# Kernel tuning notes

Measured on AMD Instinct MI355X. Metric: run time of the kernel, lower is better.

The kernel has to match this reference:

```python
import jax, jax.numpy as jnp
import numpy as np

K_NN = 64          # ume_knn
RADIUS = 1.5       # ume_desc_rad
EPS_M = 1e-6
EPS_T = 1e-16


def ball_query_idx(kp, pts, K, radius):
    # kp: [bs, n_kp, 3], pts: [bs, N, 3] -> idx [bs, n_kp, K], -1 padded
    N = pts.shape[1]
    d2 = jnp.sum((kp[:, :, None, :] - pts[:, None, :, :]) ** 2, axis=-1)  # [bs,n_kp,N]
    mask = d2 < radius ** 2
    cand = jnp.where(mask, jnp.arange(N, dtype=jnp.int32), N)
    order = jnp.sort(cand, axis=-1)[..., :K]          # first K in-ball indices (by point index)
    return jnp.where(order == N, -1, order)


def ball_query_gather(pts, idx):
    # pad row 0 with zeros so idx=-1 gathers zeros (matches torch ball_query_gather)
    bs = pts.shape[0]
    padded = jnp.concatenate([jnp.zeros((bs, 1, pts.shape[-1]), pts.dtype), pts], axis=1)
    return padded[jnp.arange(bs)[:, None, None], idx + 1]  # [bs, n_kp, K, D]


def ume_mat(points, features):
    # points: [B', K, 3], features: [B', K, F] -> [B', F, 4]
    m0 = jnp.sum(features, axis=1)                       # [B', F]
    m1 = jnp.einsum('bkf,bkd->bfd', features, points)    # [B', F, 3]
    um = jnp.concatenate([m0[:, :, None], m1], axis=2)   # [B', F, 4]
    denom = jnp.sum(m0, axis=-1)[:, None, None] + EPS_M  # [B',1,1]
    return um / denom


def batch_estimate_transform_ume(G, H):
    # G, H: [B, F, 4]
    mg, mh = G[:, :, 0:1], H[:, :, 0:1]                  # [B,F,1]
    g, h = G[:, :, 1:], H[:, :, 1:]                      # [B,F,3]
    mg_sq = jnp.sum(mg ** 2, axis=1, keepdims=True) + EPS_T
    mg_mh = jnp.sum(mg * mh, axis=1, keepdims=True)
    gmg = jnp.sum(g * mg, axis=1, keepdims=True)         # [B,1,3]
    hmg = jnp.sum(h * mg, axis=1, keepdims=True)
    wlc = gmg / (mg_sq + EPS_T)
    wrc = hmg / (mg_mh + EPS_T)
    left = g - wlc * mg
    right = h - wrc * mh
    M = jnp.einsum('bfi,bfj->bij', right, left)          # right^T @ left, [B,3,3]
    U, S, VH = jnp.linalg.svd(jnp.swapaxes(M, 1, 2))
    sgn = jnp.sign(jnp.linalg.det(U @ VH))
    qd = jnp.stack([jnp.ones_like(sgn), jnp.ones_like(sgn), sgn], axis=-1)  # diag(1,1,sgn)
    R = (U * qd[:, None, :]) @ VH                        # [B,3,3]
    b2 = (wrc - wlc @ R)[:, 0, :]                        # [B,3]
    H_orth = jnp.linalg.qr(H, mode='reduced')[0]
    G_orth = jnp.linalg.qr(G, mode='reduced')[0]
    diff = H_orth @ jnp.swapaxes(H_orth, 1, 2) - G_orth @ jnp.swapaxes(G_orth, 1, 2)
    D = 0.707 * jnp.sqrt(jnp.sum(diff ** 2, axis=(1, 2)))
    top = jnp.concatenate([jnp.swapaxes(R, 1, 2), b2[:, :, None]], axis=2)  # [B,3,4]
    bottom = jnp.broadcast_to(jnp.array([[0.0, 0.0, 0.0, 1.0]], G.dtype), (G.shape[0], 1, 4))
    T = jnp.concatenate([top, bottom], axis=1)           # [B,4,4]
    return T, D


def setup_inputs() -> dict:
    key = jax.random.key(0)
    ks = jax.random.split(key, 6)
    bs, N, F, n_kp = 2, 16384, 64, 64
    return {
        'source_points': jax.random.normal(ks[0], (bs, N, 3), jnp.float32),
        'source_features': jax.random.uniform(ks[1], (bs, N, F), jnp.float32),
        'source_kp': jax.random.normal(ks[2], (bs, n_kp, 3), jnp.float32),
        'target_points': jax.random.normal(ks[3], (bs, N, 3), jnp.float32),
        'target_features': jax.random.uniform(ks[4], (bs, N, F), jnp.float32),
        'target_kp': jax.random.normal(ks[5], (bs, n_kp, 3), jnp.float32),
    }


def reference(source_points, source_features, source_kp, target_points, target_features, target_kp):
    bs, n_kp = source_kp.shape[0], source_kp.shape[1]
    F = source_features.shape[-1]
    s_idx = ball_query_idx(source_kp, source_points, K_NN, RADIUS)
    t_idx = ball_query_idx(target_kp, target_points, K_NN, RADIUS)
    s_pts = ball_query_gather(source_points, s_idx).reshape(bs * n_kp, K_NN, 3)
    s_ft = ball_query_gather(source_features, s_idx).reshape(bs * n_kp, K_NN, F)
    t_pts = ball_query_gather(target_points, t_idx).reshape(bs * n_kp, K_NN, 3)
    t_ft = ball_query_gather(target_features, t_idx).reshape(bs * n_kp, K_NN, F)
    G_kp = ume_mat(s_pts, s_ft).reshape(bs, n_kp, F, 4)[:, :, None]   # [bs,n_kp,1,F,4]
    H_kp = ume_mat(t_pts, t_ft).reshape(bs, n_kp, F, 4)[:, None]      # [bs,1,n_kp,F,4]
    G = jnp.broadcast_to(G_kp, (bs, n_kp, n_kp, F, 4)).reshape(-1, F, 4)
    H = jnp.broadcast_to(H_kp, (bs, n_kp, n_kp, F, 4)).reshape(-1, F, 4)
    T, D = batch_estimate_transform_ume(G, H)
    T = T.reshape(bs, n_kp, n_kp, 4, 4)
    D = D.reshape(bs, n_kp, n_kp)
    return T, D, jnp.squeeze(G_kp), jnp.squeeze(H_kp)
```

## Files before the change

### kernel.cpp

```cpp
#include <hip/hip_runtime.h>
#include <math.h>

#define N_PTS 16384
#define N_KP  64
#define NF    64
#define KNN   64
#define NWAVE 16

#define OFF_T 0
#define OFF_D 131072
#define OFF_G 139264
#define OFF_H 172032

__device__ __forceinline__ float wsum(float v) {
  #pragma unroll
  for (int m = 1; m < 64; m <<= 1) v += __shfl_xor(v, m, 64);
  return v;
}

__global__ __launch_bounds__(1024) void ume_stage1(
    const float* __restrict__ sp, const float* __restrict__ sf, const float* __restrict__ skp,
    const float* __restrict__ tp, const float* __restrict__ tf, const float* __restrict__ tkp,
    float* __restrict__ out, double* __restrict__ rec)
{
  const int kp = blockIdx.x, b = blockIdx.y, side = blockIdx.z;
  const int tid  = threadIdx.x;
  const int lane = tid & 63;
  const int w    = tid >> 6;
  const float* pts  = side ? tp  : sp;
  const float* feat = side ? tf  : sf;
  const float* kps  = side ? tkp : skp;

  const float kx = kps[(b*N_KP + kp)*3 + 0];
  const float ky = kps[(b*N_KP + kp)*3 + 1];
  const float kz = kps[(b*N_KP + kp)*3 + 2];

  __shared__ int   s_widx[NWAVE*KNN];
  __shared__ float s_wpx[NWAVE*KNN], s_wpy[NWAVE*KNN], s_wpz[NWAVE*KNN];
  __shared__ int   s_wcount[NWAVE];
  __shared__ int   s_woff[NWAVE];
  __shared__ int   s_total;
  __shared__ int   s_final[KNN];
  __shared__ float s_px[KNN], s_py[KNN], s_pz[KNN];
  __shared__ float s_m0[NWAVE][NF], s_mx[NWAVE][NF], s_my[NWAVE][NF], s_mz[NWAVE][NF];

  const float* base = pts + ((size_t)b*N_PTS + w*1024 + lane)*3;
  float cx = base[0], cy = base[1], cz = base[2];
  int running = 0;
  #pragma unroll 5
  for (int k = 0; k < 15; ++k) {
    const float* q = base + (size_t)(k+1)*192;
    const float nx = q[0], ny = q[1], nz = q[2];
    const float dx = cx-kx, dy = cy-ky, dz = cz-kz;
    const bool hit = (dx*dx + dy*dy + dz*dz) < 2.25f;
    const unsigned long long m = __ballot(hit);
    if (hit) {
      const int pos = running + __popcll(m & ((1ull<<lane)-1ull));
      if (pos < KNN) {
        s_widx[w*KNN + pos] = w*1024 + k*64 + lane;
        s_wpx[w*KNN + pos] = cx; s_wpy[w*KNN + pos] = cy; s_wpz[w*KNN + pos] = cz;
      }
    }
    running += (int)__popcll(m);
    cx = nx; cy = ny; cz = nz;
  }
  {
    const float dx = cx-kx, dy = cy-ky, dz = cz-kz;
    const bool hit = (dx*dx + dy*dy + dz*dz) < 2.25f;
    const unsigned long long m = __ballot(hit);
    if (hit) {
      const int pos = running + __popcll(m & ((1ull<<lane)-1ull));
      if (pos < KNN) {
        s_widx[w*KNN + pos] = w*1024 + 15*64 + lane;
        s_wpx[w*KNN + pos] = cx; s_wpy[w*KNN + pos] = cy; s_wpz[w*KNN + pos] = cz;
      }
    }
    running += (int)__popcll(m);
  }
  if (lane == 0) s_wcount[w] = running > KNN ? KNN : running;
  __syncthreads();

  if (tid < NWAVE) {
    int off = 0;
    for (int q = 0; q < tid; ++q) off += s_wcount[q];
    s_woff[tid] = off;
    if (tid == NWAVE-1) {
      int tot = off + s_wcount[tid];
      s_total = tot > KNN ? KNN : tot;
    }
  }
  __syncthreads();

  {
    const int e = tid & 63, ww = tid >> 6;
    if (e < s_wcount[ww]) {
      const int slot = s_woff[ww] + e;
      if (slot < KNN) {
        s_final[slot] = s_widx[ww*KNN + e];
        s_px[slot] = s_wpx[ww*KNN + e];
        s_py[slot] = s_wpy[ww*KNN + e];
        s_pz[slot] = s_wpz[ww*KNN + e];
      }
    }
  }
  __syncthreads();

  const int total = s_total;

  {
    const int f = tid & 63, g = tid >> 6;
    float m0 = 0.f, mxv = 0.f, myv = 0.f, mzv = 0.f;
    #pragma unroll
    for (int t = 0; t < 4; ++t) {
      const int k = g + t*NWAVE;
      if (k < total) {
        const float fv = feat[((size_t)b*N_PTS + s_final[k])*NF + f];
        m0  += fv;
        mxv += fv * s_px[k];
        myv += fv * s_py[k];
        mzv += fv * s_pz[k];
      }
    }
    s_m0[g][f] = m0; s_mx[g][f] = mxv; s_my[g][f] = myv; s_mz[g][f] = mzv;
  }
  __syncthreads();

  if (tid >= 64) return;

  float m0 = 0.f, mxv = 0.f, myv = 0.f, mzv = 0.f;
  #pragma unroll
  for (int g = 0; g < NWAVE; ++g) {
    m0  += s_m0[g][lane];
    mxv += s_mx[g][lane];
    myv += s_my[g][lane];
    mzv += s_mz[g][lane];
  }
  const float denom = wsum(m0) + 1e-6f;
  float u[4];
  u[0] = m0/denom; u[1] = mxv/denom; u[2] = myv/denom; u[3] = mzv/denom;

  float* dst = out + (side ? OFF_H : OFF_G) + ((size_t)(b*N_KP+kp)*NF + lane)*4;
  dst[0]=u[0]; dst[1]=u[1]; dst[2]=u[2]; dst[3]=u[3];

  float A[4][4];
  #pragma unroll
  for (int c = 0; c < 4; ++c)
    #pragma unroll
    for (int d = c; d < 4; ++d) {
      const float s = wsum(u[c]*u[d]);
      A[c][d] = s; A[d][c] = s;
    }

  if (lane < 16)
    rec[(size_t)((side*2 + b)*N_KP + kp)*16 + lane] = (double)A[lane>>2][lane&3];
}

__device__ __forceinline__ void chol_inv4(const double A[4][4], double Ai[4][4], double sc[4]) {
  #pragma unroll
  for (int c = 0; c < 4; ++c) sc[c] = 1.0/sqrt(fmax(A[c][c], 1e-300));
  double Ah[4][4];
  #pragma unroll
  for (int c = 0; c < 4; ++c)
    #pragma unroll
    for (int d = 0; d < 4; ++d) Ah[c][d] = A[c][d]*sc[c]*sc[d];
  double L[4][4] = {};
  for (int c = 0; c < 4; ++c) {
    double dv = Ah[c][c];
    for (int k = 0; k < c; ++k) dv -= L[c][k]*L[c][k];
    dv = sqrt(fmax(dv, 1e-14));
    L[c][c] = dv;
    for (int r = c+1; r < 4; ++r) {
      double v = Ah[r][c];
      for (int k = 0; k < c; ++k) v -= L[r][k]*L[c][k];
      L[r][c] = v/dv;
    }
  }
  double Li[4][4] = {};
  for (int c = 0; c < 4; ++c) {
    Li[c][c] = 1.0/L[c][c];
    for (int r = c+1; r < 4; ++r) {
      double s = 0.0;
      for (int k = c; k < r; ++k) s += L[r][k]*Li[k][c];
      Li[r][c] = -s/L[r][r];
    }
  }
  for (int r = 0; r < 4; ++r)
    for (int c = 0; c < 4; ++c) {
      double s = 0.0;
      for (int k = 0; k < 4; ++k) s += Li[k][r]*Li[k][c];
      Ai[r][c] = s;
    }
}

__global__ __launch_bounds__(64) void ume_stage2(
    const float* __restrict__ gh, float* __restrict__ out,
    const double* __restrict__ rec)
{
  const int jt = blockIdx.x, it = blockIdx.y, b = blockIdx.z;
  const int lane = threadIdx.x;
  const int i = it*8 + (lane >> 3);
  const int j = jt*8 + (lane & 7);

  const float4* Gp = (const float4*)(gh + OFF_G) + (size_t)(b*N_KP + i)*NF;
  const float4* Hp = (const float4*)(gh + OFF_H) + (size_t)(b*N_KP + j)*NF;

  double X[4][4] = {};
  for (int f = 0; f < NF; ++f) {
    const float4 g = Gp[f];
    const float4 h = Hp[f];
    const double gc[4] = {(double)g.x, (double)g.y, (double)g.z, (double)g.w};
    const double hc[4] = {(double)h.x, (double)h.y, (double)h.z, (double)h.w};
    #pragma unroll
    for (int c = 0; c < 4; ++c)
      #pragma unroll
      for (int d = 0; d < 4; ++d)
        X[c][d] += hc[c]*gc[d];
  }

  double Ag[4][4], Bh[4][4];
  {
    const double* pg = rec + (size_t)(b*N_KP + i)*16;
    const double* ph = rec + (size_t)((2 + b)*N_KP + j)*16;
    #pragma unroll
    for (int k = 0; k < 16; ++k) { Ag[k>>2][k&3] = pg[k]; Bh[k>>2][k&3] = ph[k]; }
  }
  double Aig[4][4], scg[4], Bih[4][4], sch[4];
  chol_inv4(Ag, Aig, scg);
  chol_inv4(Bh, Bih, sch);

  const double dwl = Ag[0][0] + 2e-16;
  const double wl[3] = {Ag[0][1]/dwl, Ag[0][2]/dwl, Ag[0][3]/dwl};
  const double dmm = X[0][0] + 1e-16;
  double wr[3];
  wr[0] = X[1][0]/dmm; wr[1] = X[2][0]/dmm; wr[2] = X[3][0]/dmm;

  double M[3][3];
  #pragma unroll
  for (int r = 0; r < 3; ++r)
    #pragma unroll
    for (int c = 0; c < 3; ++c)
      M[r][c] = X[1+r][1+c] - wl[c]*X[1+r][0] - wr[r]*X[0][1+c] + wr[r]*wl[c]*X[0][0];

  double C[3][3];
  for (int r = 0; r < 3; ++r)
    for (int c = 0; c < 3; ++c) C[r][c] = M[c][r];

  double mmax = 0.0;
  for (int r = 0; r < 3; ++r)
    for (int c = 0; c < 3; ++c) mmax = fmax(mmax, fabs(C[r][c]));

  double R[3][3] = {{1,0,0},{0,1,0},{0,0,1}};
  if (mmax > 1e-300) {
    const double is = 1.0/mmax;
    for (int r = 0; r < 3; ++r)
      for (int c = 0; c < 3; ++c) C[r][c] *= is;
    double K[3][3];
    for (int p = 0; p < 3; ++p)
      for (int q = 0; q < 3; ++q) {
        double s = 0.0;
        for (int r = 0; r < 3; ++r) s += C[r][p]*C[r][q];
        K[p][q] = s;
      }
    double V[3][3] = {{1,0,0},{0,1,0},{0,0,1}};
    for (int sweep = 0; sweep < 5; ++sweep) {
      for (int p = 0; p < 2; ++p)
        for (int q = p+1; q < 3; ++q) {
          const double apq = K[p][q];
          if (fabs(apq) < 1e-60) continue;
          const double tau = (K[q][q] - K[p][p])/(2.0*apq);
          const double t   = (tau >= 0.0 ? 1.0 : -1.0)/(fabs(tau) + sqrt(1.0 + tau*tau));
          const double cth = 1.0/sqrt(1.0 + t*t);
          const double sth = t*cth;
          for (int k = 0; k < 3; ++k) {
            const double a = K[p][k], bb_ = K[q][k];
            K[p][k] = cth*a - sth*bb_;
            K[q][k] = sth*a + cth*bb_;
          }
          for (int k = 0; k < 3; ++k) {
            const double a = K[k][p], bb_ = K[k][q];
            K[k][p] = cth*a - sth*bb_;
            K[k][q] = sth*a + cth*bb_;
          }
          for (int k = 0; k < 3; ++k) {
            const double a = V[k][p], bb_ = V[k][q];
            V[k][p] = cth*a - sth*bb_;
            V[k][q] = sth*a + cth*bb_;
          }
        }
    }
    int o0 = 0, o1 = 1, o2 = 2;
    double e0 = K[0][0], e1 = K[1][1], e2 = K[2][2];
    if (e0 < e1) { double te=e0; e0=e1; e1=te; int to=o0; o0=o1; o1=to; }
    if (e0 < e2) { double te=e0; e0=e2; e2=te; int to=o0; o0=o2; o2=to; }
    if (e1 < e2) { double te=e1; e1=e2; e2=te; int to=o1; o1=o2; o2=to; }
    (void)e0; (void)e1; (void)e2;
    double v1[3] = {V[0][o0], V[1][o0], V[2][o0]};
    double v2[3] = {V[0][o1], V[1][o1], V[2][o1]};
    double u1[3], u2[3];
    for (int r = 0; r < 3; ++r) u1[r] = C[r][0]*v1[0] + C[r][1]*v1[1] + C[r][2]*v1[2];
    const double n1 = sqrt(u1[0]*u1[0] + u1[1]*u1[1] + u1[2]*u1[2]);
    if (n1 > 1e-150) { u1[0]/=n1; u1[1]/=n1; u1[2]/=n1; }
    else             { u1[0]=1.0; u1[1]=0.0; u1[2]=0.0; }
    for (int r = 0; r < 3; ++r) u2[r] = C[r][0]*v2[0] + C[r][1]*v2[1] + C[r][2]*v2[2];
    const double d12 = u2[0]*u1[0] + u2[1]*u1[1] + u2[2]*u1[2];
    for (int r = 0; r < 3; ++r) u2[r] -= d12*u1[r];
    const double n2 = sqrt(u2[0]*u2[0] + u2[1]*u2[1] + u2[2]*u2[2]);
    if (n2 > 1e-100) { u2[0]/=n2; u2[1]/=n2; u2[2]/=n2; }
    else {
      double t0, t1, t2;
      if (fabs(u1[0]) < 0.9) { t0=1.0; t1=0.0; t2=0.0; } else { t0=0.0; t1=1.0; t2=0.0; }
      const double dd = t0*u1[0] + t1*u1[1] + t2*u1[2];
      u2[0]=t0-dd*u1[0]; u2[1]=t1-dd*u1[1]; u2[2]=t2-dd*u1[2];
      const double nn = sqrt(u2[0]*u2[0] + u2[1]*u2[1] + u2[2]*u2[2]);
      u2[0]/=nn; u2[1]/=nn; u2[2]/=nn;
    }
    const double u3[3] = {u1[1]*u2[2]-u1[2]*u2[1], u1[2]*u2[0]-u1[0]*u2[2], u1[0]*u2[1]-u1[1]*u2[0]};
    const double v3[3] = {v1[1]*v2[2]-v1[2]*v2[1], v1[2]*v2[0]-v1[0]*v2[2], v1[0]*v2[1]-v1[1]*v2[0]};
    for (int r = 0; r < 3; ++r)
      for (int c = 0; c < 3; ++c)
        R[r][c] = u1[r]*v1[c] + u2[r]*v2[c] + u3[r]*v3[c];
  }

  double bb[3];
  for (int d = 0; d < 3; ++d)
    bb[d] = wr[d] - (wl[0]*R[0][d] + wl[1]*R[1][d] + wl[2]*R[2][d]);

  double Xh[4][4];
  for (int c = 0; c < 4; ++c)
    for (int d = 0; d < 4; ++d) Xh[c][d] = X[c][d]*sch[c]*scg[d];
  double W[4][4];
  for (int r = 0; r < 4; ++r)
    for (int c = 0; c < 4; ++c) {
      double s = 0.0;
      for (int k = 0; k < 4; ++k) s += Bih[r][k]*Xh[k][c];
      W[r][c] = s;
    }
  double tr = 0.0;
  for (int r = 0; r < 4; ++r)
    for (int c = 0; c < 4; ++c) {
      double s = 0.0;
      for (int k = 0; k < 4; ++k) s += W[r][k]*Aig[k][c];
      tr += s*Xh[r][c];
    }
  const double Dv = 0.707*sqrt(fmax(8.0 - 2.0*tr, 0.0));

  float* tptr = out + OFF_T + (size_t)((b*N_KP + i)*N_KP + j)*16;
  tptr[0]=(float)R[0][0];  tptr[1]=(float)R[1][0];  tptr[2]=(float)R[2][0];  tptr[3]=(float)bb[0];
  tptr[4]=(float)R[0][1];  tptr[5]=(float)R[1][1];  tptr[6]=(float)R[2][1];  tptr[7]=(float)bb[1];
  tptr[8]=(float)R[0][2];  tptr[9]=(float)R[1][2];  tptr[10]=(float)R[2][2]; tptr[11]=(float)bb[2];
  tptr[12]=0.f; tptr[13]=0.f; tptr[14]=0.f; tptr[15]=1.f;

  out[OFF_D + (size_t)(b*N_KP + i)*N_KP + j] = (float)Dv;
}

extern "C" void kernel_launch(void* const* d_in, const int* in_sizes, int n_in,
                              void* d_out, int out_size, void* d_ws, size_t ws_size,
                              hipStream_t stream) {
  const float* sp  = (const float*)d_in[0];
  const float* sf  = (const float*)d_in[1];
  const float* skp = (const float*)d_in[2];
  const float* tp  = (const float*)d_in[3];
  const float* tf  = (const float*)d_in[4];
  const float* tkp = (const float*)d_in[5];
  float* out = (float*)d_out;
  double* rec = (double*)d_ws;

  dim3 gA(N_KP, 2, 2);
  ume_stage1<<<gA, 1024, 0, stream>>>(sp, sf, skp, tp, tf, tkp, out, rec);
  dim3 gB(8, 8, 2);
  ume_stage2<<<gB, 64, 0, stream>>>(out, out, rec);
}
```

Before: 110.1 us.

## Scan ball query in block-wide rounds with early exit once K found

Restructures the ball query so each round has all 16 waves test a contiguous chunk of 1024 points, compacts hits into the final list with a block-wide prefix, and stops once 64 neighbours are collected. This avoids scanning all 16384 points when the ball fills early. In exchange it adds two barriers per round and drops the software-pipelined prefetch of the next point, so when few points fall in the radius it can be slower than the old single pass.

```diff
diff --git a/kernel.cpp b/kernel.cpp
--- a/kernel.cpp
+++ b/kernel.cpp
@@ -38,74 +38,51 @@
   __shared__ int   s_widx[NWAVE*KNN];
   __shared__ float s_wpx[NWAVE*KNN], s_wpy[NWAVE*KNN], s_wpz[NWAVE*KNN];
   __shared__ int   s_wcount[NWAVE];
-  __shared__ int   s_woff[NWAVE];
-  __shared__ int   s_total;
   __shared__ int   s_final[KNN];
   __shared__ float s_px[KNN], s_py[KNN], s_pz[KNN];
   __shared__ float s_m0[NWAVE][NF], s_mx[NWAVE][NF], s_my[NWAVE][NF], s_mz[NWAVE][NF];
 
-  const float* base = pts + ((size_t)b*N_PTS + w*1024 + lane)*3;
-  float cx = base[0], cy = base[1], cz = base[2];
-  int running = 0;
-  #pragma unroll 5
-  for (int k = 0; k < 15; ++k) {
-    const float* q = base + (size_t)(k+1)*192;
-    const float nx = q[0], ny = q[1], nz = q[2];
-    const float dx = cx-kx, dy = cy-ky, dz = cz-kz;
+  int base_total = 0;
+
+  for (int round = 0; round < 16; ++round) {
+    const int p = round*1024 + w*64 + lane;
+    const float* pp = pts + ((size_t)b*N_PTS + p)*3;
+    const float dx = pp[0]-kx, dy = pp[1]-ky, dz = pp[2]-kz;
     const bool hit = (dx*dx + dy*dy + dz*dz) < 2.25f;
     const unsigned long long m = __ballot(hit);
     if (hit) {
-      const int pos = running + __popcll(m & ((1ull<<lane)-1ull));
-      if (pos < KNN) {
-        s_widx[w*KNN + pos] = w*1024 + k*64 + lane;
-        s_wpx[w*KNN + pos] = cx; s_wpy[w*KNN + pos] = cy; s_wpz[w*KNN + pos] = cz;
+      const int pos = __popcll(m & ((1ull<<lane)-1ull));
+      s_widx[w*KNN + pos] = p;
+      s_wpx[w*KNN + pos] = pp[0]; s_wpy[w*KNN + pos] = pp[1]; s_wpz[w*KNN + pos] = pp[2];
+    }
+    if (lane == 0) s_wcount[w] = (int)__popcll(m);
+    __syncthreads();
+
+    int myoff = base_total, newtotal = base_total;
+    #pragma unroll
+    for (int q = 0; q < NWAVE; ++q) {
+      const int cq = s_wcount[q];
+      if (q < w) myoff += cq;
+      newtotal += cq;
+    }
+    if (newtotal > KNN) newtotal = KNN;
+
+    if (lane < s_wcount[w]) {
+      const int slot = myoff + lane;
+      if (slot < KNN) {
+        s_final[slot] = s_widx[w*KNN + lane];
+        s_px[slot] = s_wpx[w*KNN + lane];
+        s_py[slot] = s_wpy[w*KNN + lane];
+        s_pz[slot] = s_wpz[w*KNN + lane];
       }
     }
-    running += (int)__popcll(m);
-    cx = nx; cy = ny; cz = nz;
-  }
-  {
-    const float dx = cx-kx, dy = cy-ky, dz = cz-kz;
-    const bool hit = (dx*dx + dy*dy + dz*dz) < 2.25f;
-    const unsigned long long m = __ballot(hit);
-    if (hit) {
-      const int pos = running + __popcll(m & ((1ull<<lane)-1ull));
-      if (pos < KNN) {
-        s_widx[w*KNN + pos] = w*1024 + 15*64 + lane;
-        s_wpx[w*KNN + pos] = cx; s_wpy[w*KNN + pos] = cy; s_wpz[w*KNN + pos] = cz;
-      }
-    }
-    running += (int)__popcll(m);
-  }
-  if (lane == 0) s_wcount[w] = running > KNN ? KNN : running;
-  __syncthreads();
-
-  if (tid < NWAVE) {
-    int off = 0;
-    for (int q = 0; q < tid; ++q) off += s_wcount[q];
-    s_woff[tid] = off;
-    if (tid == NWAVE-1) {
-      int tot = off + s_wcount[tid];
-      s_total = tot > KNN ? KNN : tot;
-    }
-  }
-  __syncthreads();
-
-  {
-    const int e = tid & 63, ww = tid >> 6;
-    if (e < s_wcount[ww]) {
-      const int slot = s_woff[ww] + e;
-      if (slot < KNN) {
-        s_final[slot] = s_widx[ww*KNN + e];
-        s_px[slot] = s_wpx[ww*KNN + e];
-        s_py[slot] = s_wpy[ww*KNN + e];
-        s_pz[slot] = s_wpz[ww*KNN + e];
-      }
-    }
-  }
-  __syncthreads();
-
-  const int total = s_total;
+    base_total = newtotal;
+    __syncthreads();
+
+    if (base_total >= KNN) break;
+  }
+
+  const int total = base_total;
 
   {
     const int f = tid & 63, g = tid >> 6;
```

After: 117.7 us. 1.07x slower.
